# Kernel tuning notes

Measured on AMD Instinct MI355X. Metric: run time of the kernel, lower is better.

The kernel has to match this reference:

```python
import jax, jax.numpy as jnp
import numpy as np

BS, SEQ, H, OUT = 32, 64, 256, 1

def setup_inputs() -> dict:
    key = jax.random.key(0)
    ks = jax.random.split(key, 8)
    s3 = 1.0 / np.sqrt(3 * H)
    sh = 1.0 / np.sqrt(H)
    x = jax.random.normal(ks[0], (BS, SEQ, H), dtype=jnp.float32)
    # ChaoticAttention: Linear(3H -> H) scoring, softmax over seq
    Wa = jax.random.normal(ks[1], (3 * H, H), dtype=jnp.float32) * s3
    ba = jnp.zeros((H,), dtype=jnp.float32)
    # ChaoticLSTM cell: gates = context @ Wi + ht @ Wh + b, order i,f,g,o
    Wi = jax.random.normal(ks[2], (H, 4 * H), dtype=jnp.float32) * sh
    Wh = jax.random.normal(ks[3], (H, 4 * H), dtype=jnp.float32) * sh
    b = jnp.zeros((4 * H,), dtype=jnp.float32)
    # final fc: Linear(H -> OUT)
    Wf = jax.random.normal(ks[4], (H, OUT), dtype=jnp.float32) * sh
    bf = jnp.zeros((OUT,), dtype=jnp.float32)
    return {"x": x, "Wa": Wa, "ba": ba, "Wi": Wi, "Wh": Wh, "b": b, "Wf": Wf, "bf": bf}

def reference(x, Wa, ba, Wi, Wh, b, Wf, bf):
    bs, seq, hid = x.shape

    def step(carry, _):
        ht, ct = carry
        # attention over the full input sequence conditioned on (ht, ct)
        hrep = jnp.broadcast_to(ht[:, None, :], (bs, seq, hid))
        crep = jnp.broadcast_to(ct[:, None, :], (bs, seq, hid))
        feat = jnp.concatenate([x, hrep, crep], axis=-1)          # (bs, seq, 3H)
        alpha = jax.nn.softmax(feat @ Wa + ba, axis=1)            # softmax over seq
        context = jnp.sum(alpha * x, axis=1)                      # (bs, H)
        # one LSTM cell step on the context vector
        gates = context @ Wi + ht @ Wh + b                        # (bs, 4H)
        i, f, g, o = jnp.split(gates, 4, axis=-1)
        ct_new = jax.nn.sigmoid(f) * ct + jax.nn.sigmoid(i) * jnp.tanh(g)
        ht_new = jax.nn.sigmoid(o) * jnp.tanh(ct_new)
        return (ht_new, ct_new), None

    h0 = jnp.zeros((bs, hid), dtype=x.dtype)
    c0 = jnp.zeros((bs, hid), dtype=x.dtype)
    (ht, ct), _ = jax.lax.scan(step, (h0, c0), None, length=seq)
    return ht @ Wf + bf                                           # (bs, OUT)
```

## Files before the change

kernel.cpp:

```cpp
#include <hip/hip_runtime.h>

#define BSZ   32
#define SEQ   64
#define HID   256
#define G4    1024
#define NSTEP 64
#define QB    8
#define JB    32

typedef unsigned long long u64;
typedef unsigned int       u32;
typedef _Float16 h2v __attribute__((ext_vector_type(2)));

__device__ __forceinline__ u32 pk2(float lo, float hi) {
  return __builtin_bit_cast(u32, __builtin_amdgcn_cvt_pkrtz(lo, hi));
}
__device__ __forceinline__ float dot2_(u32 w, u32 h, float acc) {
#if __has_builtin(__builtin_amdgcn_fdot2)
  return __builtin_amdgcn_fdot2(__builtin_bit_cast(h2v, w),
                                __builtin_bit_cast(h2v, h), acc, false);
#else
  const h2v wv = __builtin_bit_cast(h2v, w), hv = __builtin_bit_cast(h2v, h);
  return acc + (float)wv[0] * (float)hv[0] + (float)wv[1] * (float)hv[1];
#endif
}
__device__ __forceinline__ float sigmoid_f(float x) {
  return __fdividef(1.f, 1.f + __expf(-x));
}
__device__ __forceinline__ float tanh_f(float x) {
  const float xc = fminf(fmaxf(x, -18.f), 18.f);
  const float e  = __expf(2.f * xc);
  return __fdividef(e - 1.f, e + 1.f);
}

__global__ __launch_bounds__(256, 1) void k_fused(
    const float* __restrict__ x, const float* __restrict__ Wa,
    const float* __restrict__ Wi, const float* __restrict__ Wh,
    const float* __restrict__ bias, const float* __restrict__ Wf,
    const float* __restrict__ bf,
    u64* __restrict__ tht2, u64* __restrict__ ctxT, float* __restrict__ out)
{
  const int b    = blockIdx.x & 31;
  const int q    = blockIdx.x >> 5;
  const int tid  = threadIdx.x;
  const int lane = tid & 63;
  const int wv   = tid >> 6;
  const int jq   = tid & 7;
  const int g    = (tid >> 3) & 3;
  const int kq   = tid >> 5;
  const int cq4  = g * 8 + jq;

  __shared__ __align__(16) u32   smem[26944];
  __shared__ __align__(16) u32   hs2[128];
  __shared__ __align__(16) float cs[256];
  __shared__ __align__(16) float gred[2][8][128];
  __shared__ float red[4];
  float* arena = (float*)smem;
  u32*   lds_w = smem;

  const float* xb = x + (size_t)b * SEQ * HID;

#pragma unroll
  for (int it = 0; it < 16; ++it) {
    const int gl = it * 1024 + tid * 4;
    const int s = gl >> 8, k = gl & 255;
    *(float4*)&arena[s * 260 + k] = *(const float4*)(xb + gl);
  }
#pragma unroll
  for (int it = 0; it < 8; ++it) {
    const int idx = it * 256 + tid;
    const int k = idx >> 3, cq = idx & 7;
    *(float4*)&arena[16640 + k * 32 + cq * 4] =
        *(const float4*)(Wa + (size_t)k * HID + q * JB + cq * 4);
  }
  __syncthreads();

  {
    const int ts = tid >> 2, tc = tid & 3;
    float l0 = 0.f, l1 = 0.f, l2 = 0.f, l3 = 0.f,
          l4 = 0.f, l5 = 0.f, l6 = 0.f, l7 = 0.f;
    const float* xrow = &arena[ts * 260];
    const float* wab  = &arena[16640 + tc * 8];
    for (int k4 = 0; k4 < 64; ++k4) {
      const float4 xv = *(const float4*)&xrow[k4 * 4];
#define LSTEP(XE, KO)                                                        \
      { const float4 wa = *(const float4*)&wab[(k4 * 4 + KO) * 32];          \
        const float4 wb2 = *(const float4*)&wab[(k4 * 4 + KO) * 32 + 4];     \
        l0 += (XE) * wa.x;  l1 += (XE) * wa.y;  l2 += (XE) * wa.z;           \
        l3 += (XE) * wa.w;  l4 += (XE) * wb2.x; l5 += (XE) * wb2.y;          \
        l6 += (XE) * wb2.z; l7 += (XE) * wb2.w; }
      LSTEP(xv.x, 0) LSTEP(xv.y, 1) LSTEP(xv.z, 2) LSTEP(xv.w, 3)
#undef LSTEP
    }
    float* lrow = &arena[24832 + ts * 33 + tc * 8];
    lrow[0] = l0; lrow[1] = l1; lrow[2] = l2; lrow[3] = l3;
    lrow[4] = l4; lrow[5] = l5; lrow[6] = l6; lrow[7] = l7;
  }
  __syncthreads();

  {
    const int jx = tid >> 3, sp = tid & 7;
    float lg[8];
#pragma unroll
    for (int e = 0; e < 8; ++e) lg[e] = arena[24832 + (sp * 8 + e) * 33 + jx];
    float m = lg[0];
#pragma unroll
    for (int e = 1; e < 8; ++e) m = fmaxf(m, lg[e]);
    m = fmaxf(m, __shfl_xor(m, 1));
    m = fmaxf(m, __shfl_xor(m, 2));
    m = fmaxf(m, __shfl_xor(m, 4));
    float ex[8], sm = 0.f;
#pragma unroll
    for (int e = 0; e < 8; ++e) { ex[e] = __expf(lg[e] - m); sm += ex[e]; }
    sm += __shfl_xor(sm, 1);
    sm += __shfl_xor(sm, 2);
    sm += __shfl_xor(sm, 4);
    const float inv = 1.f / sm;
    const int gj = q * JB + jx;
    float cx = 0.f;
#pragma unroll
    for (int e = 0; e < 8; ++e) cx += ex[e] * arena[(sp * 8 + e) * 260 + gj];
    cx *= inv;
    cx += __shfl_xor(cx, 1);
    cx += __shfl_xor(cx, 2);
    cx += __shfl_xor(cx, 4);
    if (sp == 0)
      __hip_atomic_store(ctxT + b * HID + gj,
                         (((u64)__float_as_uint(cx)) << 32) | 1ull,
                         __ATOMIC_RELAXED, __HIP_MEMORY_SCOPE_AGENT);
  }
  __syncthreads();

#define STAGE_W16(SRC)                                                       \
  _Pragma("unroll")                                                          \
  for (int i = 0; i < 16; ++i) {                                             \
    const int idx = i * 256 + tid;                                           \
    const int kp = idx >> 5, c4 = idx & 31;                                  \
    const int gc = (c4 >> 3) * HID + q * JB + (c4 & 7) * 4;                  \
    const float4 a  = *(const float4*)((SRC) + (size_t)(2 * kp) * G4 + gc);  \
    const float4 b2 = *(const float4*)((SRC) + (size_t)(2 * kp + 1) * G4 + gc);\
    *(uint4*)&lds_w[kp * 128 + c4 * 4] =                                     \
        make_uint4(pk2(a.x, b2.x), pk2(a.y, b2.y),                           \
                   pk2(a.z, b2.z), pk2(a.w, b2.w));                          \
  }

#define MACW(H2SRC, ACC)                                                     \
  _Pragma("unroll")                                                          \
  for (int kpl = 0; kpl < 16; ++kpl) {                                       \
    const uint4 wq = *(const uint4*)&lds_w[(kq * 16 + kpl) * 128 + cq4 * 4]; \
    const u32 h2 = (H2SRC)[kpl];                                             \
    ACC.x = dot2_(wq.x, h2, ACC.x);                                          \
    ACC.y = dot2_(wq.y, h2, ACC.y);                                          \
    ACC.z = dot2_(wq.z, h2, ACC.z);                                          \
    ACC.w = dot2_(wq.w, h2, ACC.w);                                          \
  }

  STAGE_W16(Wi)
  {
    const u64* pp = ctxT + b * HID + tid;
    u64 pk;
    do {
      pk = __hip_atomic_load(pp, __ATOMIC_RELAXED, __HIP_MEMORY_SCOPE_AGENT);
    } while ((u32)pk != 1u);
    cs[tid] = __uint_as_float((u32)(pk >> 32));
  }
  __syncthreads();

  {
    u32 ch2[16];
    const float2* cp = (const float2*)&cs[kq * 32];
#pragma unroll
    for (int i = 0; i < 16; ++i) ch2[i] = pk2(cp[i].x, cp[i].y);
    float4 ac = {0.f, 0.f, 0.f, 0.f};
    MACW(ch2, ac)
    *(float4*)&gred[0][kq][cq4 * 4] = ac;
  }
  __syncthreads();

  float4 gcr = {0.f, 0.f, 0.f, 0.f};
  float  cst = 0.f;
  if (tid < 32) {
    const int qj = q * JB + tid;
#pragma unroll
    for (int k2 = 0; k2 < 8; ++k2) {
      const float* gp = &gred[0][k2][tid];
      gcr.x += gp[0]; gcr.y += gp[32]; gcr.z += gp[64]; gcr.w += gp[96];
    }
    gcr.x += bias[qj];           gcr.y += bias[HID + qj];
    gcr.z += bias[2 * HID + qj]; gcr.w += bias[3 * HID + qj];
    const float ig = sigmoid_f(gcr.x);
    const float g2 = tanh_f(gcr.z), og = sigmoid_f(gcr.w);
    cst = ig * g2;
    const float hv = og * tanh_f(cst);
    const float hp_ = __shfl_xor(hv, 1);
    if ((tid & 1) == 0) {
      const u32 d = pk2(hv, hp_);
      __hip_atomic_store(tht2 + (size_t)BSZ * 128 + b * 128 + q * 16 + (tid >> 1),
                         (((u64)d) << 32) | 1ull,
                         __ATOMIC_RELAXED, __HIP_MEMORY_SCOPE_AGENT);
    }
  }
  STAGE_W16(Wh)
  __syncthreads();

  for (int t = 1; t < NSTEP; ++t) {
    const int rb = t & 1;
    {
      const u64* pp = tht2 + (size_t)rb * BSZ * 128 + b * 128 + (tid >> 1);
      u64 pk;
      do {
        pk = __hip_atomic_load(pp, __ATOMIC_RELAXED, __HIP_MEMORY_SCOPE_AGENT);
      } while ((u32)pk != (u32)t);
      hs2[tid >> 1] = (u32)(pk >> 32);
    }
    float4 a2 = {0.f, 0.f, 0.f, 0.f};
    {
      const u32* hp = &hs2[kq * 16];
      u32 hh[16];
#pragma unroll
      for (int i4 = 0; i4 < 4; ++i4) {
        const uint4 hq = *(const uint4*)&hp[i4 * 4];
        hh[i4 * 4 + 0] = hq.x; hh[i4 * 4 + 1] = hq.y;
        hh[i4 * 4 + 2] = hq.z; hh[i4 * 4 + 3] = hq.w;
      }
      MACW(hh, a2)
    }
    *(float4*)&gred[rb][kq][cq4 * 4] = a2;
    __syncthreads();

    if (tid < 32) {
      float4 s = gcr;
#pragma unroll
      for (int k2 = 0; k2 < 8; ++k2) {
        const float* gp = &gred[rb][k2][tid];
        s.x += gp[0]; s.y += gp[32]; s.z += gp[64]; s.w += gp[96];
      }
      const float ig = sigmoid_f(s.x), fg = sigmoid_f(s.y);
      const float g2 = tanh_f(s.z),    og = sigmoid_f(s.w);
      cst = fg * cst + ig * g2;
      const float hv = og * tanh_f(cst);
      const float hp_ = __shfl_xor(hv, 1);
      if ((tid & 1) == 0) {
        const u32 d = pk2(hv, hp_);
        __hip_atomic_store(tht2 + (size_t)((t + 1) & 1) * BSZ * 128
                               + b * 128 + q * 16 + (tid >> 1),
                           (((u64)d) << 32) | (u64)(u32)(t + 1),
                           __ATOMIC_RELAXED, __HIP_MEMORY_SCOPE_AGENT);
      }
    }
  }

  if (q == 0) {
    const u64* pp = tht2 +  b * 128 + (tid >> 1);
    u64 pk;
    do {
      pk = __hip_atomic_load(pp, __ATOMIC_RELAXED, __HIP_MEMORY_SCOPE_AGENT);
    } while ((u32)pk != (u32)NSTEP);
    const h2v hh = __builtin_bit_cast(h2v, (u32)(pk >> 32));
    const float hval = (tid & 1) ? (float)hh[1] : (float)hh[0];
    float prod = hval * Wf[tid];
#pragma unroll
    for (int mk = 1; mk < 64; mk <<= 1) prod += __shfl_xor(prod, mk);
    if (lane == 0) red[wv] = prod;
    __syncthreads();
    if (tid == 0) out[b] = red[0] + red[1] + red[2] + red[3] + bf[0];
  }
#undef MACW
#undef STAGE_W16
}

extern "C" void kernel_launch(void* const* d_in, const int* in_sizes, int n_in,
                              void* d_out, int out_size, void* d_ws, size_t ws_size,
                              hipStream_t stream)
{
  const float* x  = (const float*)d_in[0];
  const float* Wa = (const float*)d_in[1];
  const float* Wi = (const float*)d_in[3];
  const float* Wh = (const float*)d_in[4];
  const float* bi = (const float*)d_in[5];
  const float* Wf = (const float*)d_in[6];
  const float* bf = (const float*)d_in[7];
  float* out = (float*)d_out;

  u64* tht2 = (u64*)d_ws;
  u64* ctxT = (u64*)((char*)d_ws + (size_t)2 * BSZ * 128 * sizeof(u64));

  hipLaunchKernelGGL(k_fused, dim3(BSZ * QB), dim3(256), 0, stream,
                     x, Wa, Wi, Wh, bi, Wf, bf, tht2, ctxT, out);
}
```

Baseline: 179.2 us.

## Replace per-step LDS reduction and block barrier with wavefront-local shuffles

The thread mapping is reorganised so that each wavefront owns 8 hidden columns and splits the K dimension across its 8 lane groups. The K partial sums are then reduced with cross-lane shuffles instead of an LDS gred buffer and a __syncthreads. The recurrent h vector is read straight from global into registers and distributed with ds_bpermute, replacing the hs2 shared staging. This removes the block-wide barrier from the 63-step serial loop and lets wavefronts run independently, at the cost of a relayout of the staged weights and more shuffle instructions per step.

```diff
diff --git a/kernel.cpp b/kernel.cpp
--- a/kernel.cpp
+++ b/kernel.cpp
@@ -20,8 +20,8 @@
   return __builtin_amdgcn_fdot2(__builtin_bit_cast(h2v, w),
                                 __builtin_bit_cast(h2v, h), acc, false);
 #else
-  const h2v wv = __builtin_bit_cast(h2v, w), hv = __builtin_bit_cast(h2v, h);
-  return acc + (float)wv[0] * (float)hv[0] + (float)wv[1] * (float)hv[1];
+  const h2v wv_ = __builtin_bit_cast(h2v, w), hv_ = __builtin_bit_cast(h2v, h);
+  return acc + (float)wv_[0] * (float)hv_[0] + (float)wv_[1] * (float)hv_[1];
 #endif
 }
 __device__ __forceinline__ float sigmoid_f(float x) {
@@ -45,15 +45,13 @@
   const int tid  = threadIdx.x;
   const int lane = tid & 63;
   const int wv   = tid >> 6;
-  const int jq   = tid & 7;
-  const int g    = (tid >> 3) & 3;
-  const int kq   = tid >> 5;
-  const int cq4  = g * 8 + jq;
+  const int cg   = lane & 7;
+  const int kq   = lane >> 3;
+  const int jj   = wv * 8 + cg;
+  const int qj   = q * JB + jj;
 
   __shared__ __align__(16) u32   smem[26944];
-  __shared__ __align__(16) u32   hs2[128];
   __shared__ __align__(16) float cs[256];
-  __shared__ __align__(16) float gred[2][8][128];
   __shared__ float red[4];
   float* arena = (float*)smem;
   u32*   lds_w = smem;
@@ -136,24 +134,35 @@
   for (int i = 0; i < 16; ++i) {                                             \
     const int idx = i * 256 + tid;                                           \
     const int kp = idx >> 5, c4 = idx & 31;                                  \
-    const int gc = (c4 >> 3) * HID + q * JB + (c4 & 7) * 4;                  \
-    const float4 a  = *(const float4*)((SRC) + (size_t)(2 * kp) * G4 + gc);  \
-    const float4 b2 = *(const float4*)((SRC) + (size_t)(2 * kp + 1) * G4 + gc);\
-    *(uint4*)&lds_w[kp * 128 + c4 * 4] =                                     \
-        make_uint4(pk2(a.x, b2.x), pk2(a.y, b2.y),                           \
-                   pk2(a.z, b2.z), pk2(a.w, b2.w));                          \
-  }
-
-#define MACW(H2SRC, ACC)                                                     \
+    const int gg = c4 >> 3, jq = c4 & 7;                                     \
+    const float* s0 = (SRC) + (size_t)(2 * kp) * G4 + gg * HID + q * JB + jq * 4; \
+    const float4 a  = *(const float4*)s0;                                    \
+    const float4 b2 = *(const float4*)(s0 + G4);                             \
+    u32* dst = &lds_w[kp * 128 + jq * 16 + gg];                              \
+    dst[0]  = pk2(a.x, b2.x);                                                \
+    dst[4]  = pk2(a.y, b2.y);                                                \
+    dst[8]  = pk2(a.z, b2.z);                                                \
+    dst[12] = pk2(a.w, b2.w);                                                \
+  }
+
+#define MACW(HH, ACC)                                                        \
   _Pragma("unroll")                                                          \
   for (int kpl = 0; kpl < 16; ++kpl) {                                       \
-    const uint4 wq = *(const uint4*)&lds_w[(kq * 16 + kpl) * 128 + cq4 * 4]; \
-    const u32 h2 = (H2SRC)[kpl];                                             \
-    ACC.x = dot2_(wq.x, h2, ACC.x);                                          \
-    ACC.y = dot2_(wq.y, h2, ACC.y);                                          \
-    ACC.z = dot2_(wq.z, h2, ACC.z);                                          \
-    ACC.w = dot2_(wq.w, h2, ACC.w);                                          \
-  }
+    const uint4 wq = *(const uint4*)&lds_w[(kq * 16 + kpl) * 128 + jj * 4];  \
+    const u32 h2w = (HH)[kpl];                                               \
+    ACC.x = dot2_(wq.x, h2w, ACC.x);                                         \
+    ACC.y = dot2_(wq.y, h2w, ACC.y);                                         \
+    ACC.z = dot2_(wq.z, h2w, ACC.z);                                         \
+    ACC.w = dot2_(wq.w, h2w, ACC.w);                                         \
+  }
+
+#define KRED(ACC)                                                            \
+  ACC.x += __shfl_xor(ACC.x, 8);  ACC.y += __shfl_xor(ACC.y, 8);             \
+  ACC.z += __shfl_xor(ACC.z, 8);  ACC.w += __shfl_xor(ACC.w, 8);             \
+  ACC.x += __shfl_xor(ACC.x, 16); ACC.y += __shfl_xor(ACC.y, 16);            \
+  ACC.z += __shfl_xor(ACC.z, 16); ACC.w += __shfl_xor(ACC.w, 16);            \
+  ACC.x += __shfl_xor(ACC.x, 32); ACC.y += __shfl_xor(ACC.y, 32);            \
+  ACC.z += __shfl_xor(ACC.z, 32); ACC.w += __shfl_xor(ACC.w, 32);
 
   STAGE_W16(Wi)
   {
@@ -166,87 +175,71 @@
   }
   __syncthreads();
 
-  {
-    u32 ch2[16];
-    const float2* cp = (const float2*)&cs[kq * 32];
-#pragma unroll
-    for (int i = 0; i < 16; ++i) ch2[i] = pk2(cp[i].x, cp[i].y);
-    float4 ac = {0.f, 0.f, 0.f, 0.f};
-    MACW(ch2, ac)
-    *(float4*)&gred[0][kq][cq4 * 4] = ac;
-  }
-  __syncthreads();
-
   float4 gcr = {0.f, 0.f, 0.f, 0.f};
   float  cst = 0.f;
-  if (tid < 32) {
-    const int qj = q * JB + tid;
-#pragma unroll
-    for (int k2 = 0; k2 < 8; ++k2) {
-      const float* gp = &gred[0][k2][tid];
-      gcr.x += gp[0]; gcr.y += gp[32]; gcr.z += gp[64]; gcr.w += gp[96];
-    }
-    gcr.x += bias[qj];           gcr.y += bias[HID + qj];
-    gcr.z += bias[2 * HID + qj]; gcr.w += bias[3 * HID + qj];
-    const float ig = sigmoid_f(gcr.x);
-    const float g2 = tanh_f(gcr.z), og = sigmoid_f(gcr.w);
-    cst = ig * g2;
-    const float hv = og * tanh_f(cst);
-    const float hp_ = __shfl_xor(hv, 1);
-    if ((tid & 1) == 0) {
-      const u32 d = pk2(hv, hp_);
-      __hip_atomic_store(tht2 + (size_t)BSZ * 128 + b * 128 + q * 16 + (tid >> 1),
-                         (((u64)d) << 32) | 1ull,
-                         __ATOMIC_RELAXED, __HIP_MEMORY_SCOPE_AGENT);
-    }
-  }
+  {
+    u32 ch[16];
+    const float2* cp = (const float2*)&cs[kq * 32];
+#pragma unroll
+    for (int i = 0; i < 16; ++i) ch[i] = pk2(cp[i].x, cp[i].y);
+    float4 ac = {0.f, 0.f, 0.f, 0.f};
+    MACW(ch, ac)
+    KRED(ac)
+    if (kq == 0) {
+      gcr.x = ac.x + bias[qj];           gcr.y = ac.y + bias[HID + qj];
+      gcr.z = ac.z + bias[2 * HID + qj]; gcr.w = ac.w + bias[3 * HID + qj];
+      const float ig = sigmoid_f(gcr.x);
+      const float g2 = tanh_f(gcr.z), og = sigmoid_f(gcr.w);
+      cst = ig * g2;
+      const float hv = og * tanh_f(cst);
+      const float hp = __shfl_xor(hv, 1);
+      if ((cg & 1) == 0)
+        __hip_atomic_store(tht2 + (size_t)BSZ * 128 + b * 128
+                               + q * 16 + wv * 4 + (cg >> 1),
+                           (((u64)pk2(hv, hp)) << 32) | 1ull,
+                           __ATOMIC_RELAXED, __HIP_MEMORY_SCOPE_AGENT);
+    }
+  }
+  __syncthreads();
   STAGE_W16(Wh)
   __syncthreads();
 
   for (int t = 1; t < NSTEP; ++t) {
     const int rb = t & 1;
-    {
-      const u64* pp = tht2 + (size_t)rb * BSZ * 128 + b * 128 + (tid >> 1);
-      u64 pk;
-      do {
-        pk = __hip_atomic_load(pp, __ATOMIC_RELAXED, __HIP_MEMORY_SCOPE_AGENT);
-      } while ((u32)pk != (u32)t);
-      hs2[tid >> 1] = (u32)(pk >> 32);
-    }
+    const u64* pp = tht2 + (size_t)rb * BSZ * 128 + b * 128 + lane * 2;
+    u64 p0, p1;
+    do {
+      p0 = __hip_atomic_load(pp, __ATOMIC_RELAXED, __HIP_MEMORY_SCOPE_AGENT);
+    } while ((u32)p0 != (u32)t);
+    do {
+      p1 = __hip_atomic_load(pp + 1, __ATOMIC_RELAXED, __HIP_MEMORY_SCOPE_AGENT);
+    } while ((u32)p1 != (u32)t);
+    const int r0 = (int)(u32)(p0 >> 32);
+    const int r1 = (int)(u32)(p1 >> 32);
+
+    u32 hh[16];
+#pragma unroll
+    for (int i2 = 0; i2 < 8; ++i2) {
+      const int sl = (kq * 8 + i2) * 4;
+      hh[2 * i2]     = (u32)__builtin_amdgcn_ds_bpermute(sl, r0);
+      hh[2 * i2 + 1] = (u32)__builtin_amdgcn_ds_bpermute(sl, r1);
+    }
+
     float4 a2 = {0.f, 0.f, 0.f, 0.f};
-    {
-      const u32* hp = &hs2[kq * 16];
-      u32 hh[16];
-#pragma unroll
-      for (int i4 = 0; i4 < 4; ++i4) {
-        const uint4 hq = *(const uint4*)&hp[i4 * 4];
-        hh[i4 * 4 + 0] = hq.x; hh[i4 * 4 + 1] = hq.y;
-        hh[i4 * 4 + 2] = hq.z; hh[i4 * 4 + 3] = hq.w;
-      }
-      MACW(hh, a2)
-    }
-    *(float4*)&gred[rb][kq][cq4 * 4] = a2;
-    __syncthreads();
-
-    if (tid < 32) {
-      float4 s = gcr;
-#pragma unroll
-      for (int k2 = 0; k2 < 8; ++k2) {
-        const float* gp = &gred[rb][k2][tid];
-        s.x += gp[0]; s.y += gp[32]; s.z += gp[64]; s.w += gp[96];
-      }
-      const float ig = sigmoid_f(s.x), fg = sigmoid_f(s.y);
-      const float g2 = tanh_f(s.z),    og = sigmoid_f(s.w);
+    MACW(hh, a2)
+    KRED(a2)
+
+    if (kq == 0) {
+      const float ig = sigmoid_f(a2.x + gcr.x), fg = sigmoid_f(a2.y + gcr.y);
+      const float g2 = tanh_f(a2.z + gcr.z),    og = sigmoid_f(a2.w + gcr.w);
       cst = fg * cst + ig * g2;
       const float hv = og * tanh_f(cst);
-      const float hp_ = __shfl_xor(hv, 1);
-      if ((tid & 1) == 0) {
-        const u32 d = pk2(hv, hp_);
+      const float hp = __shfl_xor(hv, 1);
+      if ((cg & 1) == 0)
         __hip_atomic_store(tht2 + (size_t)((t + 1) & 1) * BSZ * 128
-                               + b * 128 + q * 16 + (tid >> 1),
-                           (((u64)d) << 32) | (u64)(u32)(t + 1),
+                               + b * 128 + q * 16 + wv * 4 + (cg >> 1),
+                           (((u64)pk2(hv, hp)) << 32) | (u64)(u32)(t + 1),
                            __ATOMIC_RELAXED, __HIP_MEMORY_SCOPE_AGENT);
-      }
     }
   }
 
@@ -256,8 +249,8 @@
     do {
       pk = __hip_atomic_load(pp, __ATOMIC_RELAXED, __HIP_MEMORY_SCOPE_AGENT);
     } while ((u32)pk != (u32)NSTEP);
-    const h2v hh = __builtin_bit_cast(h2v, (u32)(pk >> 32));
-    const float hval = (tid & 1) ? (float)hh[1] : (float)hh[0];
+    const h2v hh_ = __builtin_bit_cast(h2v, (u32)(pk >> 32));
+    const float hval = (tid & 1) ? (float)hh_[1] : (float)hh_[0];
     float prod = hval * Wf[tid];
 #pragma unroll
     for (int mk = 1; mk < 64; mk <<= 1) prod += __shfl_xor(prod, mk);
@@ -266,6 +259,7 @@
     if (tid == 0) out[b] = red[0] + red[1] + red[2] + red[3] + bf[0];
   }
 #undef MACW
+#undef KRED
 #undef STAGE_W16
 }
 
```

Result: slower. 258.1 us (+44.0%).

## Keep recurrent Wh slice in registers and parallelize gate reduction across all threads

Applied to the files above, without the earlier changes.

Loads each thread's fp16 Wh slice into 16 uint4 registers once before the recurrent loop, so the per-step matvec no longer re-reads weights from LDS. The per-step cross-k reduction of gate partials now runs across all 256 threads: 8 lanes per gate column, combined with xor shuffles, where before 32 threads each summed 8 LDS values serially. The gred row stride is padded to 132 to reduce bank conflicts. This shortens the serial critical path of each of the 64 dependent steps, at the cost of 64 extra VGPRs and shuffle work.

```diff
diff --git a/kernel.cpp b/kernel.cpp
--- a/kernel.cpp
+++ b/kernel.cpp
@@ -20,8 +20,8 @@
   return __builtin_amdgcn_fdot2(__builtin_bit_cast(h2v, w),
                                 __builtin_bit_cast(h2v, h), acc, false);
 #else
-  const h2v wv = __builtin_bit_cast(h2v, w), hv = __builtin_bit_cast(h2v, h);
-  return acc + (float)wv[0] * (float)hv[0] + (float)wv[1] * (float)hv[1];
+  const h2v wv_ = __builtin_bit_cast(h2v, w), hv_ = __builtin_bit_cast(h2v, h);
+  return acc + (float)wv_[0] * (float)hv_[0] + (float)wv_[1] * (float)hv_[1];
 #endif
 }
 __device__ __forceinline__ float sigmoid_f(float x) {
@@ -49,11 +49,15 @@
   const int g    = (tid >> 3) & 3;
   const int kq   = tid >> 5;
   const int cq4  = g * 8 + jq;
+  const int jl   = lane >> 3;
+  const int k2   = lane & 7;
+  const int jr   = wv * 8 + jl;
+  const int qjr  = q * JB + jr;
 
   __shared__ __align__(16) u32   smem[26944];
   __shared__ __align__(16) u32   hs2[128];
   __shared__ __align__(16) float cs[256];
-  __shared__ __align__(16) float gred[2][8][128];
+  __shared__ __align__(16) float gred[2][8][132];
   __shared__ float red[4];
   float* arena = (float*)smem;
   u32*   lds_w = smem;
@@ -144,17 +148,6 @@
                    pk2(a.z, b2.z), pk2(a.w, b2.w));                          \
   }
 
-#define MACW(H2SRC, ACC)                                                     \
-  _Pragma("unroll")                                                          \
-  for (int kpl = 0; kpl < 16; ++kpl) {                                       \
-    const uint4 wq = *(const uint4*)&lds_w[(kq * 16 + kpl) * 128 + cq4 * 4]; \
-    const u32 h2 = (H2SRC)[kpl];                                             \
-    ACC.x = dot2_(wq.x, h2, ACC.x);                                          \
-    ACC.y = dot2_(wq.y, h2, ACC.y);                                          \
-    ACC.z = dot2_(wq.z, h2, ACC.z);                                          \
-    ACC.w = dot2_(wq.w, h2, ACC.w);                                          \
-  }
-
   STAGE_W16(Wi)
   {
     const u64* pp = ctxT + b * HID + tid;
@@ -167,41 +160,57 @@
   __syncthreads();
 
   {
-    u32 ch2[16];
+    u32 ch[16];
     const float2* cp = (const float2*)&cs[kq * 32];
 #pragma unroll
-    for (int i = 0; i < 16; ++i) ch2[i] = pk2(cp[i].x, cp[i].y);
+    for (int i = 0; i < 16; ++i) ch[i] = pk2(cp[i].x, cp[i].y);
     float4 ac = {0.f, 0.f, 0.f, 0.f};
-    MACW(ch2, ac)
+#pragma unroll
+    for (int kpl = 0; kpl < 16; ++kpl) {
+      const uint4 wq = *(const uint4*)&lds_w[(kq * 16 + kpl) * 128 + cq4 * 4];
+      ac.x = dot2_(wq.x, ch[kpl], ac.x);
+      ac.y = dot2_(wq.y, ch[kpl], ac.y);
+      ac.z = dot2_(wq.z, ch[kpl], ac.z);
+      ac.w = dot2_(wq.w, ch[kpl], ac.w);
+    }
     *(float4*)&gred[0][kq][cq4 * 4] = ac;
   }
   __syncthreads();
 
   float4 gcr = {0.f, 0.f, 0.f, 0.f};
   float  cst = 0.f;
-  if (tid < 32) {
-    const int qj = q * JB + tid;
-#pragma unroll
-    for (int k2 = 0; k2 < 8; ++k2) {
-      const float* gp = &gred[0][k2][tid];
-      gcr.x += gp[0]; gcr.y += gp[32]; gcr.z += gp[64]; gcr.w += gp[96];
-    }
-    gcr.x += bias[qj];           gcr.y += bias[HID + qj];
-    gcr.z += bias[2 * HID + qj]; gcr.w += bias[3 * HID + qj];
-    const float ig = sigmoid_f(gcr.x);
-    const float g2 = tanh_f(gcr.z), og = sigmoid_f(gcr.w);
-    cst = ig * g2;
-    const float hv = og * tanh_f(cst);
-    const float hp_ = __shfl_xor(hv, 1);
-    if ((tid & 1) == 0) {
-      const u32 d = pk2(hv, hp_);
-      __hip_atomic_store(tht2 + (size_t)BSZ * 128 + b * 128 + q * 16 + (tid >> 1),
-                         (((u64)d) << 32) | 1ull,
-                         __ATOMIC_RELAXED, __HIP_MEMORY_SCOPE_AGENT);
+  {
+    const float* gp = &gred[0][k2][0];
+    float4 s;
+    s.x = gp[jr]; s.y = gp[32 + jr]; s.z = gp[64 + jr]; s.w = gp[96 + jr];
+    s.x += __shfl_xor(s.x, 1); s.y += __shfl_xor(s.y, 1);
+    s.z += __shfl_xor(s.z, 1); s.w += __shfl_xor(s.w, 1);
+    s.x += __shfl_xor(s.x, 2); s.y += __shfl_xor(s.y, 2);
+    s.z += __shfl_xor(s.z, 2); s.w += __shfl_xor(s.w, 2);
+    s.x += __shfl_xor(s.x, 4); s.y += __shfl_xor(s.y, 4);
+    s.z += __shfl_xor(s.z, 4); s.w += __shfl_xor(s.w, 4);
+    if (k2 == 0) {
+      gcr.x = s.x + bias[qjr];           gcr.y = s.y + bias[HID + qjr];
+      gcr.z = s.z + bias[2 * HID + qjr]; gcr.w = s.w + bias[3 * HID + qjr];
+      const float ig = sigmoid_f(gcr.x);
+      const float g2 = tanh_f(gcr.z), og = sigmoid_f(gcr.w);
+      cst = ig * g2;
+      const float hv = og * tanh_f(cst);
+      const float hp = __shfl_xor(hv, 8);
+      if ((jl & 1) == 0)
+        __hip_atomic_store(tht2 + (size_t)BSZ * 128 + b * 128
+                               + q * 16 + wv * 4 + (jl >> 1),
+                           (((u64)pk2(hv, hp)) << 32) | 1ull,
+                           __ATOMIC_RELAXED, __HIP_MEMORY_SCOPE_AGENT);
     }
   }
   STAGE_W16(Wh)
   __syncthreads();
+
+  uint4 wreg[16];
+#pragma unroll
+  for (int i = 0; i < 16; ++i)
+    wreg[i] = *(const uint4*)&lds_w[(kq * 16 + i) * 128 + cq4 * 4];
 
   for (int t = 1; t < NSTEP; ++t) {
     const int rb = t & 1;
@@ -215,37 +224,46 @@
     }
     float4 a2 = {0.f, 0.f, 0.f, 0.f};
     {
-      const u32* hp = &hs2[kq * 16];
       u32 hh[16];
+      const u32* hp_ = &hs2[kq * 16];
 #pragma unroll
       for (int i4 = 0; i4 < 4; ++i4) {
-        const uint4 hq = *(const uint4*)&hp[i4 * 4];
+        const uint4 hq = *(const uint4*)&hp_[i4 * 4];
         hh[i4 * 4 + 0] = hq.x; hh[i4 * 4 + 1] = hq.y;
         hh[i4 * 4 + 2] = hq.z; hh[i4 * 4 + 3] = hq.w;
       }
-      MACW(hh, a2)
+#pragma unroll
+      for (int kpl = 0; kpl < 16; ++kpl) {
+        a2.x = dot2_(wreg[kpl].x, hh[kpl], a2.x);
+        a2.y = dot2_(wreg[kpl].y, hh[kpl], a2.y);
+        a2.z = dot2_(wreg[kpl].z, hh[kpl], a2.z);
+        a2.w = dot2_(wreg[kpl].w, hh[kpl], a2.w);
+      }
     }
     *(float4*)&gred[rb][kq][cq4 * 4] = a2;
     __syncthreads();
 
-    if (tid < 32) {
-      float4 s = gcr;
-#pragma unroll
-      for (int k2 = 0; k2 < 8; ++k2) {
-        const float* gp = &gred[rb][k2][tid];
-        s.x += gp[0]; s.y += gp[32]; s.z += gp[64]; s.w += gp[96];
-      }
-      const float ig = sigmoid_f(s.x), fg = sigmoid_f(s.y);
-      const float g2 = tanh_f(s.z),    og = sigmoid_f(s.w);
-      cst = fg * cst + ig * g2;
-      const float hv = og * tanh_f(cst);
-      const float hp_ = __shfl_xor(hv, 1);
-      if ((tid & 1) == 0) {
-        const u32 d = pk2(hv, hp_);
-        __hip_atomic_store(tht2 + (size_t)((t + 1) & 1) * BSZ * 128
-                               + b * 128 + q * 16 + (tid >> 1),
-                           (((u64)d) << 32) | (u64)(u32)(t + 1),
-                           __ATOMIC_RELAXED, __HIP_MEMORY_SCOPE_AGENT);
+    {
+      const float* gp = &gred[rb][k2][0];
+      float4 s;
+      s.x = gp[jr]; s.y = gp[32 + jr]; s.z = gp[64 + jr]; s.w = gp[96 + jr];
+      s.x += __shfl_xor(s.x, 1); s.y += __shfl_xor(s.y, 1);
+      s.z += __shfl_xor(s.z, 1); s.w += __shfl_xor(s.w, 1);
+      s.x += __shfl_xor(s.x, 2); s.y += __shfl_xor(s.y, 2);
+      s.z += __shfl_xor(s.z, 2); s.w += __shfl_xor(s.w, 2);
+      s.x += __shfl_xor(s.x, 4); s.y += __shfl_xor(s.y, 4);
+      s.z += __shfl_xor(s.z, 4); s.w += __shfl_xor(s.w, 4);
+      if (k2 == 0) {
+        const float ig = sigmoid_f(s.x + gcr.x), fg = sigmoid_f(s.y + gcr.y);
+        const float g2 = tanh_f(s.z + gcr.z),    og = sigmoid_f(s.w + gcr.w);
+        cst = fg * cst + ig * g2;
+        const float hv = og * tanh_f(cst);
+        const float hp = __shfl_xor(hv, 8);
+        if ((jl & 1) == 0)
+          __hip_atomic_store(tht2 + (size_t)((t + 1) & 1) * BSZ * 128
+                                 + b * 128 + q * 16 + wv * 4 + (jl >> 1),
+                             (((u64)pk2(hv, hp)) << 32) | (u64)(u32)(t + 1),
+                             __ATOMIC_RELAXED, __HIP_MEMORY_SCOPE_AGENT);
       }
     }
   }
@@ -256,8 +274,8 @@
     do {
       pk = __hip_atomic_load(pp, __ATOMIC_RELAXED, __HIP_MEMORY_SCOPE_AGENT);
     } while ((u32)pk != (u32)NSTEP);
-    const h2v hh = __builtin_bit_cast(h2v, (u32)(pk >> 32));
-    const float hval = (tid & 1) ? (float)hh[1] : (float)hh[0];
+    const h2v hh_ = __builtin_bit_cast(h2v, (u32)(pk >> 32));
+    const float hval = (tid & 1) ? (float)hh_[1] : (float)hh_[0];
     float prod = hval * Wf[tid];
 #pragma unroll
     for (int mk = 1; mk < 64; mk <<= 1) prod += __shfl_xor(prod, mk);
@@ -265,7 +283,6 @@
     __syncthreads();
     if (tid == 0) out[b] = red[0] + red[1] + red[2] + red[3] + bf[0];
   }
-#undef MACW
 #undef STAGE_W16
 }
 
```

Result: slower. 201.4 us (+12.4%).
